# Kernel tuning notes

Measured on AMD Instinct MI355X. Metric: run time of the kernel, lower is better.

## Reference

```python
import jax, jax.numpy as jnp
import numpy as np

N_NODES = 50000
N_EDGES = 1000000
D_IN = 64
D_OUT = 64
N_REL = 8


def setup_inputs() -> dict:
    key = jax.random.key(0)
    ks = jax.random.split(key, 8)
    x = jax.random.normal(ks[0], (N_NODES, D_IN), dtype=jnp.float32)
    edge_src = jax.random.randint(ks[1], (N_EDGES,), 0, N_NODES, dtype=jnp.int32)
    edge_dst = jax.random.randint(ks[2], (N_EDGES,), 0, N_NODES, dtype=jnp.int32)
    edge_rel = jax.random.randint(ks[3], (N_EDGES,), 0, N_REL, dtype=jnp.int32)
    edge_weight = jnp.ones((N_EDGES,), dtype=jnp.float32)
    W_linear = jax.random.normal(ks[4], (N_REL * D_IN, D_OUT), dtype=jnp.float32) * (1.0 / np.sqrt(N_REL * D_IN))
    b_linear = jnp.zeros((D_OUT,), dtype=jnp.float32)
    W_self = jax.random.normal(ks[5], (D_IN, D_OUT), dtype=jnp.float32) * (1.0 / np.sqrt(D_IN))
    b_self = jnp.zeros((D_OUT,), dtype=jnp.float32)
    return {"x": x, "edge_src": edge_src, "edge_dst": edge_dst, "edge_rel": edge_rel,
            "edge_weight": edge_weight, "W_linear": W_linear, "b_linear": b_linear,
            "W_self": W_self, "b_self": b_self}


def reference(x, edge_src, edge_dst, edge_rel, edge_weight, W_linear, b_linear, W_self, b_self):
    N, d = x.shape
    R = W_linear.shape[0] // d
    # per-(dst, relation) segment ids, as in node_out * num_relation + relation
    seg = edge_dst * R + edge_rel  # [E]
    # degree normalization (message_and_aggregate path: no eps, divide by out-degree)
    deg = jax.ops.segment_sum(edge_weight, seg, num_segments=N * R)  # [N*R]
    ew = edge_weight / deg[seg]  # [E]
    # sparse mm: adjacency.T @ x == segment-sum of normalized gathered source features
    msg = x[edge_src] * ew[:, None]  # [E, d]
    update = jax.ops.segment_sum(msg, seg, num_segments=N * R)  # [N*R, d]
    update = update.reshape(N, R * d)
    # combine: linear(update) + self_loop(x), then relu
    out = update @ W_linear + b_linear + x @ W_self + b_self
    return jax.nn.relu(out)
```

## Files before the change

kernel.cpp:

```cpp
#include <hip/hip_runtime.h>
#include <stdint.h>

#define NNODES 50000
#define NEDGES 1000000
#define DIM    64
#define NREL   8
#define NBIN   489
#define NBINB  3125
#define NBINBP 3584
#define TPITCH 3136
#define BCAP   480
#define PITCH  592
#define PREPN  (18 * 4 * 64 * 8)

typedef __attribute__((ext_vector_type(8))) short short8;
typedef __attribute__((ext_vector_type(4))) float float4v;
typedef __attribute__((ext_vector_type(4))) unsigned short us4;

__device__ __forceinline__ unsigned short f2bf(float f) {
  unsigned int u = __float_as_uint(f);
  unsigned int r = (u + 0x7FFF + ((u >> 16) & 1)) >> 16;
  return (unsigned short)r;
}
__device__ __forceinline__ unsigned int f2fp8(float f) {
  unsigned u = __float_as_uint(f);
  unsigned s = (u >> 24) & 0x80u;
  unsigned a = u & 0x7FFFFFFFu;
  if (a < 0x3C800000u) return s;
  unsigned r = a + 0x7FFFFu + ((a >> 20) & 1u);
  return s | (((r >> 20) - 960u) & 0x7Fu);
}
__device__ __forceinline__ float fp8d(unsigned b) {
  unsigned v = ((b & 0x7Fu) << 20) + 0x3C000000u;
  unsigned s = (b & 0x80u) << 24;
  return __uint_as_float(v | s);
}

__global__ __launch_bounds__(512) void build_kernel(
    const float4* __restrict__ x4,
    const float* __restrict__ Wlin, const float* __restrict__ Wself,
    const float* __restrict__ blin, const float* __restrict__ bself,
    const int4* __restrict__ src4, const int4* __restrict__ dst4,
    const int4* __restrict__ rel4, const float4* __restrict__ w4,
    us4* __restrict__ xb, unsigned int* __restrict__ xq4,
    unsigned short* __restrict__ Bf2, float* __restrict__ bsum,
    uint2* __restrict__ staged2, unsigned short* __restrict__ tab, int E4) {
  __shared__ int lhist[NBINBP];
  __shared__ int lscan[NBINBP];
  __shared__ uint2 lrec[2048];
  __shared__ int wsumB[8];
  int tid = threadIdx.x;
  int lane = tid & 63;
  int wave = tid >> 6;
  int j = blockIdx.x;
  int gid = j * 512 + tid;
  const int TOT = NBIN * 512;

  for (int t = gid; t < NNODES * DIM / 4; t += TOT) {
    float4 v = x4[t];
    us4 o;
    o.x = f2bf(v.x); o.y = f2bf(v.y); o.z = f2bf(v.z); o.w = f2bf(v.w);
    xb[t] = o;
    xq4[t] = f2fp8(v.x) | (f2fp8(v.y) << 8) | (f2fp8(v.z) << 16) | (f2fp8(v.w) << 24);
  }
  if (gid < PREPN) {
    int t = gid;
    int jj = t & 7;
    int l  = (t >> 3) & 63;
    int ct = (t >> 9) & 3;
    int ks = t >> 11;
    int k = ks * 32 + (l >> 4) * 8 + jj;
    int c = ct * 16 + (l & 15);
    float v = (k < 512) ? Wlin[(size_t)k * 64 + c] : Wself[(size_t)(k - 512) * 64 + c];
    Bf2[t] = f2bf(v);
  }
  if (gid < 64) bsum[gid] = blin[gid] + bself[gid];

  for (int i = tid; i < NBINBP; i += 512) lhist[i] = 0;
  __syncthreads();
  bool valid = gid < E4;
  int4 s = {0,0,0,0}, d = {0,0,0,0}, r = {0,0,0,0};
  float4 w = {0.f,0.f,0.f,0.f};
  if (valid) { s = src4[gid]; d = dst4[gid]; r = rel4[gid]; w = w4[gid]; }
  int b0=0,b1=0,b2=0,b3=0,p0=0,p1=0,p2=0,p3=0;
  if (valid) {
    b0 = d.x >> 4; p0 = atomicAdd(&lhist[b0], 1);
    b1 = d.y >> 4; p1 = atomicAdd(&lhist[b1], 1);
    b2 = d.z >> 4; p2 = atomicAdd(&lhist[b2], 1);
    b3 = d.w >> 4; p3 = atomicAdd(&lhist[b3], 1);
  }
  __syncthreads();
  {
    int base7 = tid * 7;
    int l0 = lhist[base7 + 0], l1 = lhist[base7 + 1], l2 = lhist[base7 + 2],
        l3 = lhist[base7 + 3], l4 = lhist[base7 + 4], l5 = lhist[base7 + 5],
        l6 = lhist[base7 + 6];
    int c1 = l0, c2 = c1 + l1, c3 = c2 + l2, c4 = c3 + l3,
        c5 = c4 + l4, c6 = c5 + l5, s7 = c6 + l6;
    int inc = s7;
    #pragma unroll
    for (int dd = 1; dd < 64; dd <<= 1) {
      int tt = __shfl_up(inc, dd);
      if (lane >= dd) inc += tt;
    }
    if (lane == 63) wsumB[wave] = inc;
    __syncthreads();
    int off = 0;
    #pragma unroll
    for (int i = 0; i < 8; i++) { int pv = wsumB[i]; off += (i < wave) ? pv : 0; }
    int excl = off + inc - s7;
    lscan[base7 + 0] = excl;
    lscan[base7 + 1] = excl + c1;
    lscan[base7 + 2] = excl + c2;
    lscan[base7 + 3] = excl + c3;
    lscan[base7 + 4] = excl + c4;
    lscan[base7 + 5] = excl + c5;
    lscan[base7 + 6] = excl + c6;
  }
  __syncthreads();
  if (valid) {
    int q;
    unsigned k0 = (((unsigned)(d.x & 15) << 3) | (unsigned)r.x) << 23;
    unsigned k1 = (((unsigned)(d.y & 15) << 3) | (unsigned)r.y) << 23;
    unsigned k2 = (((unsigned)(d.z & 15) << 3) | (unsigned)r.z) << 23;
    unsigned k3 = (((unsigned)(d.w & 15) << 3) | (unsigned)r.w) << 23;
    q = lscan[b0] + p0; lrec[q] = make_uint2(((unsigned)s.x << 6) | k0, __float_as_uint(w.x));
    q = lscan[b1] + p1; lrec[q] = make_uint2(((unsigned)s.y << 6) | k1, __float_as_uint(w.y));
    q = lscan[b2] + p2; lrec[q] = make_uint2(((unsigned)s.z << 6) | k2, __float_as_uint(w.z));
    q = lscan[b3] + p3; lrec[q] = make_uint2(((unsigned)s.w << 6) | k3, __float_as_uint(w.w));
  }
  __syncthreads();
  for (int i = tid; i < NBINB; i += 512) {
    int c = lhist[i];
    int cc = (c < 31) ? c : 31;
    unsigned short pk = (c > 0) ? (unsigned short)((unsigned)lscan[i] | ((unsigned)cc << 11)) : (unsigned short)0;
    tab[(size_t)j * TPITCH + i] = pk;
  }
  int cntblk = NEDGES - j * 2048;
  if (cntblk > 2048) cntblk = 2048;
  uint2* myst = staged2 + (size_t)j * 2048;
  for (int i = tid; i < cntblk; i += 512)
    myst[i] = lrec[i];
}

__global__ __launch_bounds__(512, 4) void aggemm_kernel(
    const unsigned short* __restrict__ tab,
    const uint2* __restrict__ staged2,
    const unsigned char* __restrict__ xq,
    const unsigned short* __restrict__ xb,
    const unsigned short* __restrict__ Bf2,
    const float* __restrict__ bsum,
    float* __restrict__ out) {
  __shared__ __align__(16) unsigned short At[16 * PITCH];
  __shared__ short rid[512];
  __shared__ unsigned short tabcol[NBIN];
  __shared__ short runbase[NBIN];
  __shared__ uint2 sorted[BCAP];
  __shared__ int hist[512];
  __shared__ int scn[513];
  __shared__ int wsum[8];
  __shared__ int cnt_s;
  int tid = threadIdx.x;
  int lane = tid & 63;
  int wave = tid >> 6;
  int orig = blockIdx.x;
  int xcd = orig & 7;
  int lid = orig >> 3;
  int b = ((xcd < 5) ? xcd * 391 : (5 * 391 + (xcd - 5) * 390)) + lid;
  int nodeBase = b * 16;

  hist[tid] = 0;
  rid[tid] = 0;
  unsigned tv = (tid < NBIN) ? (unsigned)tab[(size_t)tid * TPITCH + b] : 0u;
  int rc = (int)(tv >> 11);
  int inc = rc;
  #pragma unroll
  for (int dd = 1; dd < 64; dd <<= 1) {
    int tt = __shfl_up(inc, dd);
    if (lane >= dd) inc += tt;
  }
  if (lane == 63) wsum[wave] = inc;
  __syncthreads();
  {
    int off = 0;
    #pragma unroll
    for (int i = 0; i < 8; i++) { int pv = wsum[i]; off += (i < wave) ? pv : 0; }
    int excl = off + inc - rc;
    if (tid < NBIN) {
      tabcol[tid] = (unsigned short)tv;
      runbase[tid] = (short)excl;
      if (rc > 0 && excl < BCAP) rid[excl] = (short)tid;
    }
    if (tid == 511) cnt_s = (off + inc < BCAP) ? (off + inc) : BCAP;
  }
  __syncthreads();
  {
    int a0 = (int)rid[tid];
    int minc = a0;
    #pragma unroll
    for (int dd = 1; dd < 64; dd <<= 1) {
      int tt = __shfl_up(minc, dd);
      if (lane >= dd) minc = max(minc, tt);
    }
    if (lane == 63) wsum[wave] = minc;
    __syncthreads();
    int moff = 0;
    #pragma unroll
    for (int i = 0; i < 8; i++) { int pv = wsum[i]; moff = (i < wave) ? max(moff, pv) : moff; }
    int ew = __shfl_up(minc, 1);
    int p = (lane > 0) ? max(moff, ew) : moff;
    rid[tid] = (short)max(p, a0);
  }
  __syncthreads();
  int cntC = cnt_s;
  uint2 g0 = make_uint2(0, 0);
  int k0 = -1;
  if (tid < cntC) {
    int jr = (int)rid[tid];
    int pp = (int)(tabcol[jr] & 0x7FFu) + tid - (int)runbase[jr];
    g0 = staged2[(size_t)jr * 2048 + pp];
    k0 = (int)(g0.x >> 23);
    atomicAdd(&hist[k0], 1);
  }
  __syncthreads();
  {
    int v = hist[tid];
    int kinc = v;
    #pragma unroll
    for (int dd = 1; dd < 64; dd <<= 1) {
      int tt = __shfl_up(kinc, dd);
      if (lane >= dd) kinc += tt;
    }
    if (lane == 63) wsum[wave] = kinc;
    __syncthreads();
    int off = 0;
    #pragma unroll
    for (int i = 0; i < 8; i++) { int pv = wsum[i]; off += (i < wave) ? pv : 0; }
    scn[tid] = off + kinc - v;
    if (tid == 511) scn[512] = off + kinc;
    hist[tid] = off + kinc - v;
  }
  __syncthreads();
  if (k0 >= 0) { int pq = atomicAdd(&hist[k0], 1); sorted[pq] = g0; }
  __syncthreads();

  {
    unsigned int* az0 = (unsigned int*)(At + (wave * 2) * PITCH);
    unsigned int* az1 = (unsigned int*)(At + (wave * 2 + 1) * PITCH);
    #pragma unroll
    for (int z = 0; z < 4; z++) { az0[z * 64 + lane] = 0u; az1[z * 64 + lane] = 0u; }
  }
  {
    int kbase = wave * 16;
    int s0 = scn[kbase];
    int E0 = scn[kbase + 16];
    int Em1 = (E0 > 0) ? (E0 - 1) : 0;
    int curkey = -1;
    float A = 0.f, S = 0.f;
    #define LD1(i, AX, WY) { int ii = e + (i); ii = (ii < E0) ? ii : Em1; \
      uint2 t = sorted[ii]; AX = t.x; WY = t.y; }
    #define GA1(AX, V) { V = (unsigned)xq[((AX) & 0x3FFFC0u) + (unsigned)lane]; }
    #define FLUSHK { float rd = (S != 0.f) ? (1.0f / S) : 0.f; \
      At[(curkey >> 3) * PITCH + (curkey & 7) * 64 + lane] = f2bf(A * rd); }
    #define AC1(i, AX, WY, V) { bool val = (e + (i) < E0); \
      unsigned kx = (unsigned)__builtin_amdgcn_readfirstlane((int)(AX)); \
      int kj = (int)(kx >> 23); \
      float wj = val ? __uint_as_float(WY) : 0.f; \
      if (val && kj != curkey) { if (curkey >= 0) FLUSHK; curkey = kj; A = 0.f; S = 0.f; } \
      A += wj * fp8d(V); S += wj; }
    for (int e = s0; e < E0; e += 8) {
      unsigned ax0, ax1, ax2, ax3, ax4, ax5, ax6, ax7;
      unsigned wy0, wy1, wy2, wy3, wy4, wy5, wy6, wy7;
      unsigned v0, v1, v2, v3, v4, v5, v6, v7;
      LD1(0, ax0, wy0) LD1(1, ax1, wy1) LD1(2, ax2, wy2) LD1(3, ax3, wy3)
      LD1(4, ax4, wy4) LD1(5, ax5, wy5) LD1(6, ax6, wy6) LD1(7, ax7, wy7)
      GA1(ax0, v0) GA1(ax1, v1) GA1(ax2, v2) GA1(ax3, v3)
      GA1(ax4, v4) GA1(ax5, v5) GA1(ax6, v6) GA1(ax7, v7)
      AC1(0, ax0, wy0, v0) AC1(1, ax1, wy1, v1)
      AC1(2, ax2, wy2, v2) AC1(3, ax3, wy3, v3)
      AC1(4, ax4, wy4, v4) AC1(5, ax5, wy5, v5)
      AC1(6, ax6, wy6, v6) AC1(7, ax7, wy7, v7)
    }
    if (curkey >= 0) FLUSHK
    #undef LD1
    #undef GA1
    #undef AC1
    #undef FLUSHK
  }
  {
    int node0 = nodeBase + wave * 2;
    At[(wave * 2) * PITCH + 512 + lane]     = xb[(size_t)node0 * 64 + lane];
    At[(wave * 2 + 1) * PITCH + 512 + lane] = xb[(size_t)(node0 + 1) * 64 + lane];
  }
  __syncthreads();

  if (wave < 4) {
    int m = lane & 15;
    int q = lane >> 4;
    float4v o4 = {0.f, 0.f, 0.f, 0.f};
    const short8* Bp = (const short8*)Bf2;
    #pragma unroll
    for (int ks = 0; ks < 18; ks++) {
      short8 a = *(const short8*)(At + m * PITCH + ks * 32 + q * 8);
      short8 bfr = Bp[(ks * 4 + wave) * 64 + lane];
      o4 = __builtin_amdgcn_mfma_f32_16x16x32_bf16(a, bfr, o4, 0, 0, 0);
    }
    int c = wave * 16 + m;
    float bias = bsum[c];
    #pragma unroll
    for (int rr2 = 0; rr2 < 4; rr2++) {
      out[(size_t)(nodeBase + q * 4 + rr2) * 64 + c] = fmaxf(o4[rr2] + bias, 0.0f);
    }
  }
}

extern "C" void kernel_launch(void* const* d_in, const int* in_sizes, int n_in,
                              void* d_out, int out_size, void* d_ws, size_t ws_size,
                              hipStream_t stream) {
  const float* x     = (const float*)d_in[0];
  const int*   esrc  = (const int*)d_in[1];
  const int*   edst  = (const int*)d_in[2];
  const int*   erel  = (const int*)d_in[3];
  const float* ew    = (const float*)d_in[4];
  const float* Wlin  = (const float*)d_in[5];
  const float* blin  = (const float*)d_in[6];
  const float* Wself = (const float*)d_in[7];
  const float* bself = (const float*)d_in[8];
  float* out = (float*)d_out;

  char* ws = (char*)d_ws;
  size_t off = 0;
  auto alloc = [&](size_t bytes) -> void* {
    void* p = ws + off;
    off += (bytes + 255) & ~(size_t)255;
    return p;
  };
  uint2*          staged2 = (uint2*)alloc((size_t)NBIN * 2048 * sizeof(uint2));
  unsigned short* tab     = (unsigned short*)alloc((size_t)NBIN * TPITCH * sizeof(unsigned short));
  unsigned short* Bf2     = (unsigned short*)alloc((size_t)PREPN * sizeof(unsigned short));
  float*          bsum    = (float*)alloc(64 * sizeof(float));
  unsigned short* xb      = (unsigned short*)alloc((size_t)NNODES * DIM * sizeof(unsigned short));
  unsigned char*  xq      = (unsigned char*)alloc((size_t)NNODES * DIM);

  const int E4 = NEDGES / 4;
  build_kernel<<<NBIN, 512, 0, stream>>>((const float4*)x, Wlin, Wself, blin, bself,
                                         (const int4*)esrc, (const int4*)edst,
                                         (const int4*)erel, (const float4*)ew,
                                         (us4*)xb, (unsigned int*)xq, Bf2, bsum,
                                         staged2, tab, E4);
  aggemm_kernel<<<NBINB, 512, 0, stream>>>(tab, staged2, xq, xb, Bf2, bsum, out);
}
```

Before: 144.6 us.

## Aggregate gathered edge features with MFMA instead of serial per-edge scalar accumulation

The per-wave segment reduction over sorted edges is recast as a small matrix multiply. A one-hot weight matrix (edge key equals row) in bf16 is multiplied by the gathered fp8 source features, which are decoded into bf16 pairs. Degree sums come from a second MFMA against a ones vector. Each wave's edge range is padded to multiples of 32 in a larger zero-initialised sorted buffer. This replaces the serial readfirstlane key-change logic and scattered flushes. In exchange it adds padding work and bf16 rounding of the edge weights, and the fixed 736-entry buffer could overflow if the per-wave padding exceeds it.

```diff
diff --git a/kernel.cpp b/kernel.cpp
--- a/kernel.cpp
+++ b/kernel.cpp
@@ -10,6 +10,7 @@
 #define NBINBP 3584
 #define TPITCH 3136
 #define BCAP   480
+#define BCAP2  736
 #define PITCH  592
 #define PREPN  (18 * 4 * 64 * 8)
 
@@ -30,10 +31,13 @@
   unsigned r = a + 0x7FFFFu + ((a >> 20) & 1u);
   return s | (((r >> 20) - 960u) & 0x7Fu);
 }
-__device__ __forceinline__ float fp8d(unsigned b) {
-  unsigned v = ((b & 0x7Fu) << 20) + 0x3C000000u;
-  unsigned s = (b & 0x80u) << 24;
-  return __uint_as_float(v | s);
+__device__ __forceinline__ unsigned dec2(unsigned x) {
+  return (((x & 0x007F007Fu) << 4) + 0x3C003C00u) | ((x & 0x00800080u) << 8);
+}
+__device__ __forceinline__ unsigned pkbf(float lo, float hi) {
+  unsigned r;
+  asm("v_cvt_pk_bf16_f32 %0, %1, %2" : "=v"(r) : "v"(lo), "v"(hi));
+  return r;
 }
 
 __global__ __launch_bounds__(512) void build_kernel(
@@ -155,10 +159,11 @@
   __shared__ short rid[512];
   __shared__ unsigned short tabcol[NBIN];
   __shared__ short runbase[NBIN];
-  __shared__ uint2 sorted[BCAP];
+  __shared__ uint2 sorted[BCAP2];
   __shared__ int hist[512];
   __shared__ int scn[513];
   __shared__ int wsum[8];
+  __shared__ int wbase_s[8];
   __shared__ int cnt_s;
   int tid = threadIdx.x;
   int lane = tid & 63;
@@ -171,6 +176,8 @@
 
   hist[tid] = 0;
   rid[tid] = 0;
+  sorted[tid] = make_uint2(0u, 0u);
+  if (tid < BCAP2 - 512) sorted[512 + tid] = make_uint2(0u, 0u);
   unsigned tv = (tid < NBIN) ? (unsigned)tab[(size_t)tid * TPITCH + b] : 0u;
   int rc = (int)(tv >> 11);
   int inc = rc;
@@ -238,54 +245,97 @@
     for (int i = 0; i < 8; i++) { int pv = wsum[i]; off += (i < wave) ? pv : 0; }
     scn[tid] = off + kinc - v;
     if (tid == 511) scn[512] = off + kinc;
-    hist[tid] = off + kinc - v;
-  }
+  }
+  __syncthreads();
+  if (wave == 0) {
+    int Lw = (lane < 8) ? (scn[lane * 16 + 16] - scn[lane * 16]) : 0;
+    int pw = (Lw + 31) & ~31;
+    int inc2 = pw;
+    #pragma unroll
+    for (int dd = 1; dd < 8; dd <<= 1) {
+      int tt = __shfl_up(inc2, dd);
+      if (lane >= dd) inc2 += tt;
+    }
+    if (lane < 8) wbase_s[lane] = inc2 - pw;
+  }
+  __syncthreads();
+  if (tid < 128) hist[tid] = wbase_s[tid >> 4] + scn[tid] - scn[tid & ~15];
   __syncthreads();
   if (k0 >= 0) { int pq = atomicAdd(&hist[k0], 1); sorted[pq] = g0; }
   __syncthreads();
 
   {
-    unsigned int* az0 = (unsigned int*)(At + (wave * 2) * PITCH);
-    unsigned int* az1 = (unsigned int*)(At + (wave * 2 + 1) * PITCH);
-    #pragma unroll
-    for (int z = 0; z < 4; z++) { az0[z * 64 + lane] = 0u; az1[z * 64 + lane] = 0u; }
-  }
-  {
-    int kbase = wave * 16;
-    int s0 = scn[kbase];
-    int E0 = scn[kbase + 16];
-    int Em1 = (E0 > 0) ? (E0 - 1) : 0;
-    int curkey = -1;
-    float A = 0.f, S = 0.f;
-    #define LD1(i, AX, WY) { int ii = e + (i); ii = (ii < E0) ? ii : Em1; \
-      uint2 t = sorted[ii]; AX = t.x; WY = t.y; }
-    #define GA1(AX, V) { V = (unsigned)xq[((AX) & 0x3FFFC0u) + (unsigned)lane]; }
-    #define FLUSHK { float rd = (S != 0.f) ? (1.0f / S) : 0.f; \
-      At[(curkey >> 3) * PITCH + (curkey & 7) * 64 + lane] = f2bf(A * rd); }
-    #define AC1(i, AX, WY, V) { bool val = (e + (i) < E0); \
-      unsigned kx = (unsigned)__builtin_amdgcn_readfirstlane((int)(AX)); \
-      int kj = (int)(kx >> 23); \
-      float wj = val ? __uint_as_float(WY) : 0.f; \
-      if (val && kj != curkey) { if (curkey >= 0) FLUSHK; curkey = kj; A = 0.f; S = 0.f; } \
-      A += wj * fp8d(V); S += wj; }
-    for (int e = s0; e < E0; e += 8) {
-      unsigned ax0, ax1, ax2, ax3, ax4, ax5, ax6, ax7;
-      unsigned wy0, wy1, wy2, wy3, wy4, wy5, wy6, wy7;
-      unsigned v0, v1, v2, v3, v4, v5, v6, v7;
-      LD1(0, ax0, wy0) LD1(1, ax1, wy1) LD1(2, ax2, wy2) LD1(3, ax3, wy3)
-      LD1(4, ax4, wy4) LD1(5, ax5, wy5) LD1(6, ax6, wy6) LD1(7, ax7, wy7)
-      GA1(ax0, v0) GA1(ax1, v1) GA1(ax2, v2) GA1(ax3, v3)
-      GA1(ax4, v4) GA1(ax5, v5) GA1(ax6, v6) GA1(ax7, v7)
-      AC1(0, ax0, wy0, v0) AC1(1, ax1, wy1, v1)
-      AC1(2, ax2, wy2, v2) AC1(3, ax3, wy3, v3)
-      AC1(4, ax4, wy4, v4) AC1(5, ax5, wy5, v5)
-      AC1(6, ax6, wy6, v6) AC1(7, ax7, wy7, v7)
-    }
-    if (curkey >= 0) FLUSHK
-    #undef LD1
-    #undef GA1
-    #undef AC1
-    #undef FLUSHK
+    int Lw = scn[wave * 16 + 16] - scn[wave * 16];
+    int base0 = wbase_s[wave];
+    int nch = (Lw + 31) >> 5;
+    int fl = lane & 15;
+    int q8 = (lane >> 4) * 8;
+    int mg = wave * 16 + fl;
+    float4v acc0 = {0.f,0.f,0.f,0.f}, acc1 = {0.f,0.f,0.f,0.f};
+    float4v acc2 = {0.f,0.f,0.f,0.f}, acc3 = {0.f,0.f,0.f,0.f};
+    float4v accS = {0.f,0.f,0.f,0.f};
+    union U8 { short8 s8; unsigned u[4]; };
+    U8 onesf;
+    onesf.u[0] = 0x3F803F80u; onesf.u[1] = 0x3F803F80u;
+    onesf.u[2] = 0x3F803F80u; onesf.u[3] = 0x3F803F80u;
+    for (int c = 0; c < nch; c++) {
+      int rb = base0 + c * 32 + q8;
+      uint2 r0 = sorted[rb + 0], r1 = sorted[rb + 1], r2 = sorted[rb + 2], r3 = sorted[rb + 3];
+      uint2 r4 = sorted[rb + 4], r5 = sorted[rb + 5], r6 = sorted[rb + 6], r7 = sorted[rb + 7];
+      float w0 = ((int)(r0.x >> 23) == mg) ? __uint_as_float(r0.y) : 0.f;
+      float w1 = ((int)(r1.x >> 23) == mg) ? __uint_as_float(r1.y) : 0.f;
+      float w2 = ((int)(r2.x >> 23) == mg) ? __uint_as_float(r2.y) : 0.f;
+      float w3 = ((int)(r3.x >> 23) == mg) ? __uint_as_float(r3.y) : 0.f;
+      float w4 = ((int)(r4.x >> 23) == mg) ? __uint_as_float(r4.y) : 0.f;
+      float w5 = ((int)(r5.x >> 23) == mg) ? __uint_as_float(r5.y) : 0.f;
+      float w6 = ((int)(r6.x >> 23) == mg) ? __uint_as_float(r6.y) : 0.f;
+      float w7 = ((int)(r7.x >> 23) == mg) ? __uint_as_float(r7.y) : 0.f;
+      U8 af;
+      af.u[0] = pkbf(w0, w1); af.u[1] = pkbf(w2, w3);
+      af.u[2] = pkbf(w4, w5); af.u[3] = pkbf(w6, w7);
+      unsigned o0 = (r0.x & 0x3FFFC0u) + (unsigned)fl;
+      unsigned o1 = (r1.x & 0x3FFFC0u) + (unsigned)fl;
+      unsigned o2 = (r2.x & 0x3FFFC0u) + (unsigned)fl;
+      unsigned o3 = (r3.x & 0x3FFFC0u) + (unsigned)fl;
+      unsigned o4 = (r4.x & 0x3FFFC0u) + (unsigned)fl;
+      unsigned o5 = (r5.x & 0x3FFFC0u) + (unsigned)fl;
+      unsigned o6 = (r6.x & 0x3FFFC0u) + (unsigned)fl;
+      unsigned o7 = (r7.x & 0x3FFFC0u) + (unsigned)fl;
+      unsigned b00 = xq[o0],      b10 = xq[o1],      b20 = xq[o2],      b30 = xq[o3];
+      unsigned b40 = xq[o4],      b50 = xq[o5],      b60 = xq[o6],      b70 = xq[o7];
+      unsigned b01 = xq[o0 + 16], b11 = xq[o1 + 16], b21 = xq[o2 + 16], b31 = xq[o3 + 16];
+      unsigned b41 = xq[o4 + 16], b51 = xq[o5 + 16], b61 = xq[o6 + 16], b71 = xq[o7 + 16];
+      unsigned b02 = xq[o0 + 32], b12 = xq[o1 + 32], b22 = xq[o2 + 32], b32 = xq[o3 + 32];
+      unsigned b42 = xq[o4 + 32], b52 = xq[o5 + 32], b62 = xq[o6 + 32], b72 = xq[o7 + 32];
+      unsigned b03 = xq[o0 + 48], b13 = xq[o1 + 48], b23 = xq[o2 + 48], b33 = xq[o3 + 48];
+      unsigned b43 = xq[o4 + 48], b53 = xq[o5 + 48], b63 = xq[o6 + 48], b73 = xq[o7 + 48];
+      U8 bf0, bf1, bf2v, bf3v;
+      bf0.u[0]  = dec2(b00 | (b10 << 16)); bf0.u[1]  = dec2(b20 | (b30 << 16));
+      bf0.u[2]  = dec2(b40 | (b50 << 16)); bf0.u[3]  = dec2(b60 | (b70 << 16));
+      bf1.u[0]  = dec2(b01 | (b11 << 16)); bf1.u[1]  = dec2(b21 | (b31 << 16));
+      bf1.u[2]  = dec2(b41 | (b51 << 16)); bf1.u[3]  = dec2(b61 | (b71 << 16));
+      bf2v.u[0] = dec2(b02 | (b12 << 16)); bf2v.u[1] = dec2(b22 | (b32 << 16));
+      bf2v.u[2] = dec2(b42 | (b52 << 16)); bf2v.u[3] = dec2(b62 | (b72 << 16));
+      bf3v.u[0] = dec2(b03 | (b13 << 16)); bf3v.u[1] = dec2(b23 | (b33 << 16));
+      bf3v.u[2] = dec2(b43 | (b53 << 16)); bf3v.u[3] = dec2(b63 | (b73 << 16));
+      acc0 = __builtin_amdgcn_mfma_f32_16x16x32_bf16(af.s8, bf0.s8,  acc0, 0, 0, 0);
+      acc1 = __builtin_amdgcn_mfma_f32_16x16x32_bf16(af.s8, bf1.s8,  acc1, 0, 0, 0);
+      acc2 = __builtin_amdgcn_mfma_f32_16x16x32_bf16(af.s8, bf2v.s8, acc2, 0, 0, 0);
+      acc3 = __builtin_amdgcn_mfma_f32_16x16x32_bf16(af.s8, bf3v.s8, acc3, 0, 0, 0);
+      accS = __builtin_amdgcn_mfma_f32_16x16x32_bf16(af.s8, onesf.s8, accS, 0, 0, 0);
+    }
+    int rowg = lane >> 4;
+    #pragma unroll
+    for (int reg = 0; reg < 4; reg++) {
+      int lk = rowg * 4 + reg;
+      float S = accS[reg];
+      float rd = (S != 0.f) ? (1.0f / S) : 0.f;
+      int rowo = (wave * 2 + (lk >> 3)) * PITCH + (lk & 7) * 64 + fl;
+      At[rowo +  0] = f2bf(acc0[reg] * rd);
+      At[rowo + 16] = f2bf(acc1[reg] * rd);
+      At[rowo + 32] = f2bf(acc2[reg] * rd);
+      At[rowo + 48] = f2bf(acc3[reg] * rd);
+    }
   }
   {
     int node0 = nodeBase + wave * 2;
```

Result: faster. 133.7 us (-7.5%).
